# Kernel tuning notes

Measured on AMD Instinct MI355X. Metric: run time of the kernel, lower is better.

The kernel has to match this reference:

```python
import jax, jax.numpy as jnp
import numpy as np

N_NODES = 30000
N_REL = 8
N_EDGES = 131072
IN_FEAT = 512
OUT_FEAT = 512


def setup_inputs() -> dict:
    key = jax.random.key(0)
    k1, k2, k3, k4, k5 = jax.random.split(key, 5)
    x = jax.random.normal(k1, (N_NODES, IN_FEAT), dtype=jnp.float32)
    # per-relation weights [R, in, out] (xavier-ish scale)
    weight = jax.random.normal(k2, (N_REL, IN_FEAT, OUT_FEAT), dtype=jnp.float32) * (2.0 / (IN_FEAT + OUT_FEAT)) ** 0.5
    loop_weight = jax.random.normal(k3, (IN_FEAT, OUT_FEAT), dtype=jnp.float32) * (2.0 / (IN_FEAT + OUT_FEAT)) ** 0.5
    h_bias = jnp.zeros((OUT_FEAT,), dtype=jnp.float32)
    src = jax.random.randint(k4, (N_REL, N_EDGES), 0, N_NODES, dtype=jnp.int32)
    dst = jax.random.randint(k5, (N_REL, N_EDGES), 0, N_NODES, dtype=jnp.int32)
    return {"x": x, "weight": weight, "loop_weight": loop_weight,
            "h_bias": h_bias, "src": src, "dst": dst}


def reference(x, weight, loop_weight, h_bias, src, dst):
    # Per-relation GraphConv(norm='right', weight=W_r):
    #   transform all node feats, gather on src, scatter-sum on dst,
    #   normalize by in-degree (clamped to 1). Relations summed (HeteroGraphConv 'sum').
    xw = jnp.einsum('ni,rio->rno', x, weight)  # [R, N, out]

    def per_rel(xw_r, src_r, dst_r):
        msgs = xw_r[src_r]  # [E, out] gathered messages
        agg = jax.ops.segment_sum(msgs, dst_r, num_segments=N_NODES)
        deg = jax.ops.segment_sum(jnp.ones_like(dst_r, dtype=xw_r.dtype), dst_r,
                                  num_segments=N_NODES)
        return agg / jnp.clip(deg, 1.0)[:, None]

    h = jax.vmap(per_rel)(xw, src, dst).sum(axis=0)  # [N, out]
    h = h + x @ loop_weight + h_bias  # self-loop + bias
    return jax.nn.relu(h)  # activation; dropout=0.0 -> identity
```

## Files before the change

### kernel.cpp

```cpp
#include <hip/hip_runtime.h>
#include <hip/hip_bf16.h>

#define N_NODES 30000
#define N_REL   8
#define N_EDGES 131072
#define FEAT    512
#define KTOT    4608
#define CAP     32

typedef __attribute__((ext_vector_type(8))) __bf16 v8bf;
typedef __attribute__((ext_vector_type(4))) __bf16 v4bf;
typedef __attribute__((ext_vector_type(4))) float  v4f;
typedef __attribute__((ext_vector_type(8))) unsigned short u16x8;

static __device__ __forceinline__ void load_lds16(const void* g, void* l) {
  __builtin_amdgcn_global_load_lds(
      (const __attribute__((address_space(1))) void*)g,
      (__attribute__((address_space(3))) void*)l, 16, 0, 0);
}

#define CONV_BLOCKS 15000
#define TR_BLOCKS   2304
#define CNT_BLOCKS  512
__global__ __launch_bounds__(256)
void k_prep(const float* __restrict__ x, const float* __restrict__ w,
            const float* __restrict__ lw, const int* __restrict__ src,
            const int* __restrict__ dst, __bf16* __restrict__ xbf,
            __bf16* __restrict__ Wt, int* __restrict__ cnt,
            unsigned short* __restrict__ slots) {
  __shared__ float t[32][33];
  const int b = blockIdx.x, tid = threadIdx.x;
  if (b < CONV_BLOCKS) {
    int i = b * 256 + tid;
    float4 v = ((const float4*)x)[i];
    v4bf o;
    o[0] = (__bf16)v.x; o[1] = (__bf16)v.y; o[2] = (__bf16)v.z; o[3] = (__bf16)v.w;
    ((v4bf*)xbf)[i] = o;
  } else if (b < CONV_BLOCKS + TR_BLOCKS) {
    int tb = b - CONV_BLOCKS;
    int k0 = (tb % 144) * 32, n0 = (tb / 144) * 32;
    int tx = tid & 31, ty = tid >> 5;
    #pragma unroll
    for (int q = 0; q < 4; ++q) {
      int k = k0 + ty + q * 8, n = n0 + tx;
      float v = (k < 4096) ? w[(size_t)k * 512 + n] : lw[(size_t)(k - 4096) * 512 + n];
      t[ty + q * 8][tx] = v;
    }
    __syncthreads();
    #pragma unroll
    for (int q = 0; q < 4; ++q) {
      int n = n0 + ty + q * 8, k = k0 + tx;
      Wt[(size_t)n * KTOT + k] = (__bf16)t[tx][ty + q * 8];
    }
  } else {
    int cb  = b - CONV_BLOCKS - TR_BLOCKS;
    int rel = cb & 7;
    int q   = cb >> 3;
    int e0  = rel * N_EDGES + (q * 256 + tid) * 8;
    int4 sa = *(const int4*)(src + e0), sb = *(const int4*)(src + e0 + 4);
    int4 da = *(const int4*)(dst + e0), db = *(const int4*)(dst + e0 + 4);
    int ss[8] = {sa.x, sa.y, sa.z, sa.w, sb.x, sb.y, sb.z, sb.w};
    int dd[8] = {da.x, da.y, da.z, da.w, db.x, db.y, db.z, db.w};
    int bb[8], pp[8];
    #pragma unroll
    for (int j = 0; j < 8; ++j) {
      bb[j] = rel * N_NODES + dd[j];
      pp[j] = atomicAdd(&cnt[bb[j]], 1);
    }
    #pragma unroll
    for (int j = 0; j < 8; ++j)
      if (pp[j] < CAP) slots[(size_t)bb[j] * CAP + pp[j]] = (unsigned short)ss[j];
  }
}

__global__ __launch_bounds__(256)
void k_aggregate(const __bf16* __restrict__ xbf, const int* __restrict__ cnt,
                 const unsigned short* __restrict__ slots,
                 __bf16* __restrict__ out, int nBuckets) {
  int w = (blockIdx.x * blockDim.x + threadIdx.x) >> 6;
  int lane = threadIdx.x & 63;
  if (w >= nBuckets) return;
  const unsigned short* sl = slots + (size_t)w * CAP;
  u16x8 qs[4];
  qs[0] = __builtin_nontemporal_load((const u16x8*)(sl));
  qs[1] = __builtin_nontemporal_load((const u16x8*)(sl + 8));
  qs[2] = __builtin_nontemporal_load((const u16x8*)(sl + 16));
  qs[3] = __builtin_nontemporal_load((const u16x8*)(sl + 24));
  int c = __builtin_nontemporal_load(cnt + w);
  int cc = c < CAP ? c : CAP;
  const __bf16* xb = xbf + (size_t)lane * 8;
  float acc[8] = {0.f,0.f,0.f,0.f,0.f,0.f,0.f,0.f};
  #pragma unroll
  for (int g = 0; g < 4; ++g) {
    if (cc > g * 8) {
      int m = cc - g * 8;
      v8bf r[8];
      #pragma unroll
      for (int j = 0; j < 8; ++j)
        if (m > j) r[j] = *(const v8bf*)(xb + (size_t)qs[g][j] * FEAT);
      #pragma unroll
      for (int j = 0; j < 8; ++j)
        if (m > j) {
          #pragma unroll
          for (int t = 0; t < 8; ++t) acc[t] += (float)r[j][t];
        }
    }
  }
  float scale = 1.0f / (float)(c > 1 ? c : 1);
  v8bf o;
  #pragma unroll
  for (int t = 0; t < 8; ++t) o[t] = (__bf16)(acc[t] * scale);
  __builtin_nontemporal_store(o, (v8bf*)(out + (size_t)w * FEAT + lane * 8));
}

template <bool ACCUM, bool FINAL>
__global__ __launch_bounds__(256, 4)
void k_gemm(const __bf16* __restrict__ A, size_t slabStride,
            const __bf16* __restrict__ Wt, int wtStride, int kTiles,
            const float* __restrict__ bias, float* __restrict__ C,
            int mtBase, int mtEnd) {
  __shared__ __align__(16) char smem[33792];
  __bf16* As = (__bf16*)smem;
  __bf16* Bs = (__bf16*)(smem + 16384);

  const int tid  = threadIdx.x;
  const int wave = tid >> 6;
  const int lane = tid & 63;
  const int lr = lane >> 3, lc = lane & 7;
  const int gcs = (lc ^ lr) * 8;
  const int quad = lane >> 4, l15 = lane & 15;
  const int wRow = wave >> 1, wCol = wave & 1;

  const int panel = blockIdx.x >> 5;
  const int w32   = blockIdx.x & 31;
  const int mtile = mtBase + panel * 8 + (w32 & 7);
  const int ntile = w32 >> 3;
  if (mtile >= mtEnd) return;
  const int mBase = mtile * 128;
  const int nBase = ntile * 128;

  v4f acc[4][4];
  #pragma unroll
  for (int i = 0; i < 4; ++i)
    #pragma unroll
    for (int j = 0; j < 4; ++j) acc[i][j] = (v4f){0.f, 0.f, 0.f, 0.f};

  for (int kt = 0; kt < kTiles; ++kt) {
    const int kk = kt * 64;
    const __bf16* aT = A + (size_t)(kk >> 9) * slabStride + (kk & 511);
    #pragma unroll
    for (int t = 0; t < 4; ++t) {
      int chunk = wave * 4 + t;
      int row = mBase + chunk * 8 + lr;
      if (row > N_NODES - 1) row = N_NODES - 1;
      load_lds16(aT + (size_t)row * FEAT + gcs, As + chunk * 512);
      int n = nBase + chunk * 8 + lr;
      load_lds16(Wt + (size_t)n * wtStride + kk + gcs, Bs + chunk * 512);
    }
    __syncthreads();
    #pragma unroll
    for (int ks = 0; ks < 2; ++ks) {
      const int q = ks * 4 + quad;
      v8bf af[4], bfr[4];
      #pragma unroll
      for (int mi = 0; mi < 4; ++mi) {
        int m = wRow * 64 + mi * 16 + l15;
        af[mi] = *(const v8bf*)(As + m * 64 + ((q ^ (m & 7)) * 8));
      }
      #pragma unroll
      for (int ni = 0; ni < 4; ++ni) {
        int n = wCol * 64 + ni * 16 + l15;
        bfr[ni] = *(const v8bf*)(Bs + n * 64 + ((q ^ (n & 7)) * 8));
      }
      #pragma unroll
      for (int mi = 0; mi < 4; ++mi)
        #pragma unroll
        for (int ni = 0; ni < 4; ++ni)
          acc[mi][ni] = __builtin_amdgcn_mfma_f32_16x16x32_bf16(af[mi], bfr[ni], acc[mi][ni], 0, 0, 0);
    }
    __syncthreads();
  }

  float* cbuf = (float*)smem;
  const int f4c  = tid & 31;
  const int colg = nBase + f4c * 4;
  v4f bias4 = (v4f){0.f, 0.f, 0.f, 0.f};
  if (FINAL) bias4 = *(const v4f*)(bias + colg);
  #pragma unroll
  for (int h = 0; h < 2; ++h) {
    if (wRow == h) {
      #pragma unroll
      for (int mi = 0; mi < 4; ++mi) {
        int r0 = mi * 16 + quad * 4;
        #pragma unroll
        for (int ni = 0; ni < 4; ++ni) {
          int c = wCol * 64 + ni * 16 + l15;
          #pragma unroll
          for (int e = 0; e < 4; ++e)
            cbuf[(r0 + e) * 132 + c] = acc[mi][ni][e];
        }
      }
    }
    __syncthreads();
    #pragma unroll
    for (int i = 0; i < 8; ++i) {
      int rh  = (tid >> 5) + 8 * i;
      int row = mBase + h * 64 + rh;
      if (row < N_NODES) {
        v4f v = *(const v4f*)(cbuf + rh * 132 + f4c * 4);
        size_t idx = (size_t)row * FEAT + colg;
        if (ACCUM) {
          v4f c0 = *(const v4f*)(C + idx);
          v += c0;
        }
        if (FINAL) {
          #pragma unroll
          for (int e = 0; e < 4; ++e) v[e] = fmaxf(v[e] + bias4[e], 0.f);
        }
        *(v4f*)(C + idx) = v;
      }
    }
    __syncthreads();
  }
}

extern "C" void kernel_launch(void* const* d_in, const int* in_sizes, int n_in,
                              void* d_out, int out_size, void* d_ws, size_t ws_size,
                              hipStream_t stream) {
  const float* x    = (const float*)d_in[0];
  const float* w    = (const float*)d_in[1];
  const float* lw   = (const float*)d_in[2];
  const float* bias = (const float*)d_in[3];
  const int*   src  = (const int*)d_in[4];
  const int*   dst  = (const int*)d_in[5];
  float* out = (float*)d_out;

  char* ws = (char*)d_ws;
  const size_t SLAB  = (size_t)N_NODES * FEAT;
  const size_t slabB = SLAB * 2;
  const size_t wtB   = (size_t)FEAT * KTOT * 2;
  const size_t cntB  = (size_t)N_REL * N_NODES * 4;
  const size_t slotB = (size_t)N_REL * N_NODES * CAP * 2;
  const size_t fixedB = wtB + cntB + slotB;

  __bf16*         Wt     = (__bf16*)ws;
  int*            cnt    = (int*)(ws + wtB);
  unsigned short* slots  = (unsigned short*)(ws + wtB + cntB);
  __bf16*         slabs  = (__bf16*)(ws + fixedB);

  int nSlab = (int)((ws_size - fixedB) / slabB);
  int g = nSlab - 1;
  if (g > 7) g = 7;
  if (g < 1) g = 1;
  __bf16* xbf = slabs + (size_t)g * SLAB;

  hipMemsetAsync(cnt, 0, cntB, stream);
  k_prep<<<CONV_BLOCKS + TR_BLOCKS + CNT_BLOCKS, 256, 0, stream>>>(
      x, w, lw, src, dst, xbf, Wt, cnt, slots);

  const int nMtiles = (N_NODES + 127) / 128;
  const int gemmGrid = ((nMtiles + 7) / 8) * 32;

  if (g == 7) {
    k_aggregate<<<(7 * N_NODES) / 4, 256, 0, stream>>>(xbf, cnt, slots,
                                                       slabs, 7 * N_NODES);
    k_gemm<false, false><<<gemmGrid, 256, 0, stream>>>(
        slabs, SLAB, Wt, KTOT, 3584 / 64, bias, out, 0, nMtiles);
    k_aggregate<<<N_NODES / 4, 256, 0, stream>>>(
        xbf, cnt + 7 * N_NODES, slots + (size_t)7 * N_NODES * CAP,
        slabs + (size_t)6 * SLAB, N_NODES);
    k_gemm<true, true><<<gemmGrid, 256, 0, stream>>>(
        slabs + (size_t)6 * SLAB, SLAB, Wt + 3584, KTOT, 1024 / 64,
        bias, out, 0, nMtiles);
  } else {
    for (int r0 = 0; r0 < N_REL; r0 += g) {
      int gc2 = (N_REL - r0) < g ? (N_REL - r0) : g;
      k_aggregate<<<(gc2 * N_NODES) / 4, 256, 0, stream>>>(
          xbf, cnt + r0 * N_NODES, slots + (size_t)r0 * N_NODES * CAP,
          slabs, gc2 * N_NODES);
      if (r0 == 0)
        k_gemm<false, false><<<gemmGrid, 256, 0, stream>>>(
            slabs, SLAB, Wt + r0 * 512, KTOT, gc2 * 8, bias, out, 0, nMtiles);
      else
        k_gemm<true, false><<<gemmGrid, 256, 0, stream>>>(
            slabs, SLAB, Wt + r0 * 512, KTOT, gc2 * 8, bias, out, 0, nMtiles);
    }
    k_gemm<true, true><<<gemmGrid, 256, 0, stream>>>(xbf, SLAB, Wt + 4096, KTOT,
                                                     8, bias, out, 0, nMtiles);
  }
}
```

Baseline: 542.9 us.

## Add 256x256-tile ping-pong GEMM kernel with 8 waves and XCD-aware tile mapping

Adds a new GEMM kernel that uses 512 threads and 256x256 output tiles with a 128 KB double-buffered LDS. Each k-step is split into four quadrant phases, with prefetch of the next tile interleaved through barriers and s_setprio. Blocks are remapped across XCDs, and the kernel replaces the older 128-tile GEMM on the main path. The aggregate kernel also drops its nontemporal loads and stores in favour of plain accesses. The larger tiles aim to raise data reuse and MFMA utilisation, at the cost of lower occupancy, more idle blocks from tail padding (30000 rows is not a multiple of 256), and a fragile hand-written waitcnt schedule.

```diff
diff --git a/kernel.cpp b/kernel.cpp
--- a/kernel.cpp
+++ b/kernel.cpp
@@ -82,11 +82,11 @@
   if (w >= nBuckets) return;
   const unsigned short* sl = slots + (size_t)w * CAP;
   u16x8 qs[4];
-  qs[0] = __builtin_nontemporal_load((const u16x8*)(sl));
-  qs[1] = __builtin_nontemporal_load((const u16x8*)(sl + 8));
-  qs[2] = __builtin_nontemporal_load((const u16x8*)(sl + 16));
-  qs[3] = __builtin_nontemporal_load((const u16x8*)(sl + 24));
-  int c = __builtin_nontemporal_load(cnt + w);
+  qs[0] = *(const u16x8*)(sl);
+  qs[1] = *(const u16x8*)(sl + 8);
+  qs[2] = *(const u16x8*)(sl + 16);
+  qs[3] = *(const u16x8*)(sl + 24);
+  int c = cnt[w];
   int cc = c < CAP ? c : CAP;
   const __bf16* xb = xbf + (size_t)lane * 8;
   float acc[8] = {0.f,0.f,0.f,0.f,0.f,0.f,0.f,0.f};
@@ -110,7 +110,219 @@
   v8bf o;
   #pragma unroll
   for (int t = 0; t < 8; ++t) o[t] = (__bf16)(acc[t] * scale);
-  __builtin_nontemporal_store(o, (v8bf*)(out + (size_t)w * FEAT + lane * 8));
+  *(v8bf*)(out + (size_t)w * FEAT + lane * 8) = o;
+}
+
+template <bool ACCUM, bool FINAL>
+__global__ __launch_bounds__(512, 2)
+void k_gemm3(const __bf16* __restrict__ A, size_t slabStride,
+             const __bf16* __restrict__ Wt, int kTiles,
+             const float* __restrict__ bias, float* __restrict__ C) {
+  __shared__ __align__(16) char smem[131072];
+
+  const int tid  = threadIdx.x;
+  const int wave = tid >> 6, lane = tid & 63;
+  const int lr = lane >> 3, lc = lane & 7;
+  const int gcs = (lc ^ lr) * 8;
+  const int quad = lane >> 4, l15 = lane & 15;
+  const int wR2 = wave >> 2;
+  const int wC4 = wave & 3;
+
+  const int nwg = gridDim.x;
+  const int qq = nwg >> 3, rr = nwg & 7;
+  const int xcd = blockIdx.x & 7, oidx = blockIdx.x >> 3;
+  const int wg = (xcd < rr ? xcd * (qq + 1) : rr * (qq + 1) + (xcd - rr) * qq) + oidx;
+  const int mtile = wg >> 1, ntile = wg & 1;
+  const int mBase = mtile * 256, nBase = ntile * 256;
+
+  v4f acc[2][2][4][2];
+  #pragma unroll
+  for (int a = 0; a < 2; ++a)
+    #pragma unroll
+    for (int bq = 0; bq < 2; ++bq)
+      #pragma unroll
+      for (int mi = 0; mi < 4; ++mi)
+        #pragma unroll
+        for (int ni = 0; ni < 2; ++ni)
+          acc[a][bq][mi][ni] = (v4f){0.f, 0.f, 0.f, 0.f};
+
+  auto stageA = [&](int t, int h) {
+    __bf16* dst = (__bf16*)(smem + (t & 1) * 65536);
+    const int kk = t * 64;
+    const __bf16* base = A + (size_t)(kk >> 9) * slabStride + (kk & 511);
+    #pragma unroll
+    for (int r2 = 0; r2 < 2; ++r2) {
+      int rt = h * 128 + r2 * 64 + wave * 8;
+      int row = mBase + rt + lr;
+      if (row > N_NODES - 1) row = N_NODES - 1;
+      load_lds16(base + (size_t)row * FEAT + gcs, dst + rt * 64);
+    }
+  };
+  auto stageB = [&](int t, int h) {
+    __bf16* dst = (__bf16*)(smem + (t & 1) * 65536 + 32768);
+    const int kk = t * 64;
+    #pragma unroll
+    for (int r2 = 0; r2 < 2; ++r2) {
+      int rt = h * 128 + r2 * 64 + wave * 8;
+      int n = nBase + rt + lr;
+      load_lds16(Wt + (size_t)n * KTOT + kk + gcs, dst + rt * 64);
+    }
+  };
+
+  stageA(0, 0); stageB(0, 0); stageB(0, 1); stageA(0, 1);
+  asm volatile("s_waitcnt vmcnt(4)" ::: "memory");
+  __builtin_amdgcn_s_barrier();
+  __builtin_amdgcn_sched_barrier(0);
+
+  for (int t = 0; t < kTiles; ++t) {
+    const __bf16* sA = (const __bf16*)(smem + (t & 1) * 65536);
+    const __bf16* sB = sA + 16384;
+    const bool pf = (t + 1) < kTiles;
+    v8bf af[4][2], bf0[2][2], bf1[2][2];
+
+    #pragma unroll
+    for (int mi = 0; mi < 4; ++mi)
+      #pragma unroll
+      for (int ks = 0; ks < 2; ++ks) {
+        int m = wR2 * 64 + mi * 16 + l15;
+        int q = ks * 4 + quad;
+        af[mi][ks] = *(const v8bf*)(sA + m * 64 + ((q ^ (m & 7)) * 8));
+      }
+    #pragma unroll
+    for (int ni = 0; ni < 2; ++ni)
+      #pragma unroll
+      for (int ks = 0; ks < 2; ++ks) {
+        int n = wC4 * 32 + ni * 16 + l15;
+        int q = ks * 4 + quad;
+        bf0[ni][ks] = *(const v8bf*)(sB + n * 64 + ((q ^ (n & 7)) * 8));
+      }
+    if (pf) stageA(t + 1, 0);
+    __builtin_amdgcn_s_barrier();
+    asm volatile("s_waitcnt lgkmcnt(0)" ::: "memory");
+    __builtin_amdgcn_sched_barrier(0);
+    __builtin_amdgcn_s_setprio(1);
+    #pragma unroll
+    for (int ks = 0; ks < 2; ++ks)
+      #pragma unroll
+      for (int mi = 0; mi < 4; ++mi)
+        #pragma unroll
+        for (int ni = 0; ni < 2; ++ni)
+          acc[0][0][mi][ni] = __builtin_amdgcn_mfma_f32_16x16x32_bf16(
+              af[mi][ks], bf0[ni][ks], acc[0][0][mi][ni], 0, 0, 0);
+    __builtin_amdgcn_s_setprio(0);
+    if (pf) asm volatile("s_waitcnt vmcnt(4)" ::: "memory");
+    else    asm volatile("s_waitcnt vmcnt(2)" ::: "memory");
+    __builtin_amdgcn_s_barrier();
+    __builtin_amdgcn_sched_barrier(0);
+
+    #pragma unroll
+    for (int ni = 0; ni < 2; ++ni)
+      #pragma unroll
+      for (int ks = 0; ks < 2; ++ks) {
+        int n = 128 + wC4 * 32 + ni * 16 + l15;
+        int q = ks * 4 + quad;
+        bf1[ni][ks] = *(const v8bf*)(sB + n * 64 + ((q ^ (n & 7)) * 8));
+      }
+    if (pf) stageB(t + 1, 0);
+    __builtin_amdgcn_s_barrier();
+    asm volatile("s_waitcnt lgkmcnt(0)" ::: "memory");
+    __builtin_amdgcn_sched_barrier(0);
+    __builtin_amdgcn_s_setprio(1);
+    #pragma unroll
+    for (int ks = 0; ks < 2; ++ks)
+      #pragma unroll
+      for (int mi = 0; mi < 4; ++mi)
+        #pragma unroll
+        for (int ni = 0; ni < 2; ++ni)
+          acc[0][1][mi][ni] = __builtin_amdgcn_mfma_f32_16x16x32_bf16(
+              af[mi][ks], bf1[ni][ks], acc[0][1][mi][ni], 0, 0, 0);
+    __builtin_amdgcn_s_setprio(0);
+    if (pf) asm volatile("s_waitcnt vmcnt(4)" ::: "memory");
+    else    asm volatile("s_waitcnt vmcnt(0)" ::: "memory");
+    __builtin_amdgcn_s_barrier();
+    __builtin_amdgcn_sched_barrier(0);
+
+    #pragma unroll
+    for (int mi = 0; mi < 4; ++mi)
+      #pragma unroll
+      for (int ks = 0; ks < 2; ++ks) {
+        int m = 128 + wR2 * 64 + mi * 16 + l15;
+        int q = ks * 4 + quad;
+        af[mi][ks] = *(const v8bf*)(sA + m * 64 + ((q ^ (m & 7)) * 8));
+      }
+    if (pf) stageB(t + 1, 1);
+    __builtin_amdgcn_s_barrier();
+    asm volatile("s_waitcnt lgkmcnt(0)" ::: "memory");
+    __builtin_amdgcn_sched_barrier(0);
+    __builtin_amdgcn_s_setprio(1);
+    #pragma unroll
+    for (int ks = 0; ks < 2; ++ks)
+      #pragma unroll
+      for (int mi = 0; mi < 4; ++mi)
+        #pragma unroll
+        for (int ni = 0; ni < 2; ++ni)
+          acc[1][1][mi][ni] = __builtin_amdgcn_mfma_f32_16x16x32_bf16(
+              af[mi][ks], bf1[ni][ks], acc[1][1][mi][ni], 0, 0, 0);
+    __builtin_amdgcn_s_setprio(0);
+    __builtin_amdgcn_s_barrier();
+    __builtin_amdgcn_sched_barrier(0);
+
+    if (pf) stageA(t + 1, 1);
+    __builtin_amdgcn_s_barrier();
+    __builtin_amdgcn_s_setprio(1);
+    #pragma unroll
+    for (int ks = 0; ks < 2; ++ks)
+      #pragma unroll
+      for (int mi = 0; mi < 4; ++mi)
+        #pragma unroll
+        for (int ni = 0; ni < 2; ++ni)
+          acc[1][0][mi][ni] = __builtin_amdgcn_mfma_f32_16x16x32_bf16(
+              af[mi][ks], bf0[ni][ks], acc[1][0][mi][ni], 0, 0, 0);
+    __builtin_amdgcn_s_setprio(0);
+    if (pf) asm volatile("s_waitcnt vmcnt(4)" ::: "memory");
+    __builtin_amdgcn_s_barrier();
+    __builtin_amdgcn_sched_barrier(0);
+  }
+
+  asm volatile("s_waitcnt vmcnt(0)" ::: "memory");
+  float* cbuf = (float*)smem;
+  const int f4 = tid & 63;
+  const int colg = nBase + f4 * 4;
+  v4f bias4 = (v4f){0.f, 0.f, 0.f, 0.f};
+  if (FINAL) bias4 = *(const v4f*)(bias + colg);
+  #pragma unroll
+  for (int h = 0; h < 4; ++h) {
+    __syncthreads();
+    if (wR2 == (h & 1)) {
+      const int R = h >> 1;
+      #pragma unroll
+      for (int Cq = 0; Cq < 2; ++Cq)
+        #pragma unroll
+        for (int mi = 0; mi < 4; ++mi)
+          #pragma unroll
+          for (int ni = 0; ni < 2; ++ni)
+            #pragma unroll
+            for (int e = 0; e < 4; ++e)
+              cbuf[(mi * 16 + quad * 4 + e) * 260 + Cq * 128 + wC4 * 32 + ni * 16 + l15] =
+                  acc[R][Cq][mi][ni][e];
+    }
+    __syncthreads();
+    #pragma unroll
+    for (int i = 0; i < 8; ++i) {
+      int rl  = i * 8 + (tid >> 6);
+      int row = mBase + h * 64 + rl;
+      if (row < N_NODES) {
+        v4f v = *(const v4f*)(cbuf + rl * 260 + f4 * 4);
+        size_t idx = (size_t)row * FEAT + colg;
+        if (ACCUM) v += *(const v4f*)(C + idx);
+        if (FINAL) {
+          #pragma unroll
+          for (int e = 0; e < 4; ++e) v[e] = fmaxf(v[e] + bias4[e], 0.f);
+        }
+        *(v4f*)(C + idx) = v;
+      }
+    }
+  }
 }
 
 template <bool ACCUM, bool FINAL>
@@ -209,10 +421,7 @@
       if (row < N_NODES) {
         v4f v = *(const v4f*)(cbuf + rh * 132 + f4c * 4);
         size_t idx = (size_t)row * FEAT + colg;
-        if (ACCUM) {
-          v4f c0 = *(const v4f*)(C + idx);
-          v += c0;
-        }
+        if (ACCUM) v += *(const v4f*)(C + idx);
         if (FINAL) {
           #pragma unroll
           for (int e = 0; e < 4; ++e) v[e] = fmaxf(v[e] + bias4[e], 0.f);
@@ -258,21 +467,21 @@
   k_prep<<<CONV_BLOCKS + TR_BLOCKS + CNT_BLOCKS, 256, 0, stream>>>(
       x, w, lw, src, dst, xbf, Wt, cnt, slots);
 
-  const int nMtiles = (N_NODES + 127) / 128;
-  const int gemmGrid = ((nMtiles + 7) / 8) * 32;
-
   if (g == 7) {
+    const int mt256 = (N_NODES + 255) / 256;
+    const int grid3 = mt256 * 2;
     k_aggregate<<<(7 * N_NODES) / 4, 256, 0, stream>>>(xbf, cnt, slots,
                                                        slabs, 7 * N_NODES);
-    k_gemm<false, false><<<gemmGrid, 256, 0, stream>>>(
-        slabs, SLAB, Wt, KTOT, 3584 / 64, bias, out, 0, nMtiles);
+    k_gemm3<false, false><<<grid3, 512, 0, stream>>>(
+        slabs, SLAB, Wt, 3584 / 64, bias, out);
     k_aggregate<<<N_NODES / 4, 256, 0, stream>>>(
         xbf, cnt + 7 * N_NODES, slots + (size_t)7 * N_NODES * CAP,
         slabs + (size_t)6 * SLAB, N_NODES);
-    k_gemm<true, true><<<gemmGrid, 256, 0, stream>>>(
-        slabs + (size_t)6 * SLAB, SLAB, Wt + 3584, KTOT, 1024 / 64,
-        bias, out, 0, nMtiles);
+    k_gemm3<true, true><<<grid3, 512, 0, stream>>>(
+        slabs + (size_t)6 * SLAB, SLAB, Wt + 3584, 1024 / 64, bias, out);
   } else {
+    const int nMtiles = (N_NODES + 127) / 128;
+    const int gemmGrid = ((nMtiles + 7) / 8) * 32;
     for (int r0 = 0; r0 < N_REL; r0 += g) {
       int gc2 = (N_REL - r0) < g ? (N_REL - r0) : g;
       k_aggregate<<<(gc2 * N_NODES) / 4, 256, 0, stream>>>(
```

Result: faster. 528.2 us (-2.7%).
